# Optimization experiments

Measured on AMD Instinct MI355X. Metric: run time of the kernel, lower is better.

## Reference

```python
import jax, jax.numpy as jnp
import numpy as np
from jax import lax

KERNEL = 3
CIN = 512
FMAPS = 512
LATENT = 512
GAIN = 1.0
LRMUL = 1.0
# StyleGAN2 wscale: runtime_coef = gain / sqrt(fan_in) * lrmul
RC_W = GAIN / np.sqrt(KERNEL * KERNEL * CIN) * LRMUL
RC_S = GAIN / np.sqrt(LATENT) * LRMUL


def setup_inputs() -> dict:
    key = jax.random.key(0)
    k1, k2, k3, k4, k5 = jax.random.split(key, 5)
    N, H, W = 8, 64, 64
    x = jax.random.normal(k1, (N, CIN, H, W), dtype=jnp.float32)
    dlatent_vect = jax.random.normal(k2, (N, LATENT), dtype=jnp.float32)
    weight = jax.random.normal(k3, (KERNEL, KERNEL, CIN, FMAPS), dtype=jnp.float32)
    mod_weight = jax.random.normal(k4, (LATENT, CIN), dtype=jnp.float32)
    mod_bias = jax.random.normal(k5, (CIN,), dtype=jnp.float32)
    return {"x": x, "dlatent_vect": dlatent_vect, "weight": weight,
            "mod_weight": mod_weight, "mod_bias": mod_bias}


def reference(x, dlatent_vect, weight, mod_weight, mod_bias):
    N, _, H, W = x.shape
    w = weight * RC_W                                       # [kh,kw,Cin,Cout]
    # style: s = A(dlatent) + 1
    s = dlatent_vect @ (mod_weight * RC_S) + mod_bias * LRMUL + 1.0  # [N,Cin]
    # per-sample modulated weights
    ww = w[None] * s[:, None, None, :, None]                # [N,kh,kw,Cin,Cout]
    # demodulate
    d = lax.rsqrt(jnp.sum(jnp.square(ww), axis=(1, 2, 3)) + 1e-8)  # [N,Cout]
    ww = ww * d[:, None, None, None, :]
    # fused modconv: one grouped conv with N groups
    xr = x.reshape(1, N * CIN, H, W)
    wr = jnp.transpose(ww, (1, 2, 3, 0, 4)).reshape(KERNEL, KERNEL, CIN, N * FMAPS)
    out = lax.conv_general_dilated(
        xr, wr, window_strides=(1, 1), padding="SAME",
        dimension_numbers=("NCHW", "HWIO", "NCHW"),
        feature_group_count=N)
    return out.reshape(N, FMAPS, H, W)
```

## Files before the change

### kernel.cpp

```cpp
#include <hip/hip_runtime.h>
#include <math.h>

#define CIN_    512
#define COUT_   512
#define LATENT_ 512
#define NB_     8
#define HH_     64
#define WW_     64

typedef float f32x16 __attribute__((ext_vector_type(16)));
typedef short bf16x8v __attribute__((ext_vector_type(8)));

__device__ inline unsigned short f2bf(float f) {
    union { float f; unsigned u; } v; v.f = f;
    unsigned r = v.u + 0x7fffu + ((v.u >> 16) & 1u);
    return (unsigned short)(r >> 16);
}

__device__ __forceinline__ void gl_lds16(const void* g, void* l) {
    __builtin_amdgcn_global_load_lds(
        (const __attribute__((address_space(1))) unsigned int*)g,
        (__attribute__((address_space(3))) unsigned int*)l,
        16, 0, 0);
}

__global__ __launch_bounds__(256) void prep1(
    const float* __restrict__ w, const float* __restrict__ dlat,
    const float* __restrict__ mw, const float* __restrict__ mb,
    float* __restrict__ wsq, unsigned short* __restrict__ wb,
    float* __restrict__ s)
{
    __shared__ float smem[16 * 521];
    const float RC_W = 0.0147313912747197f;
    const float RC_S = 0.0441941738241592f;
    int b = blockIdx.x;
    int t = threadIdx.x;

    if (b < 1024) {
        int idx = b * 256 + t;
        float acc = 0.f;
#pragma unroll
        for (int tap = 0; tap < 9; ++tap) {
            float v = w[tap * (CIN_ * COUT_) + idx];
            acc += v * v;
        }
        wsq[idx] = acc;
    } else if (b < 1312) {
        int bb  = b - 1024;
        int tap = bb / 32;
        int cb  = bb % 32;
        for (int idx = t; idx < 16 * 512; idx += 256) {
            int ci = idx >> 9;
            int co = idx & 511;
            smem[ci * 521 + co] = w[((size_t)tap * 512 + cb * 16 + ci) * 512 + co];
        }
        __syncthreads();
        unsigned short* dst = wb + (size_t)(tap * 32 + cb) * 512 * 16;
        for (int idx = t; idx < 16 * 512; idx += 256) {
            int co = idx >> 4;
            int ci = idx & 15;
            dst[idx] = f2bf(smem[ci * 521 + co] * RC_W);
        }
    } else {
        int bb  = b - 1312;
        int n   = bb >> 3;
        int ci0 = (bb & 7) * 64;
        for (int i = t; i < LATENT_; i += 256) smem[i] = dlat[n * LATENT_ + i];
        __syncthreads();
        int cil  = t & 63;
        int part = t >> 6;
        const float* mwp = mw + ci0 + cil;
        float a0 = 0.f, a1 = 0.f;
        int l0 = part * 128;
#pragma unroll 4
        for (int l = l0; l < l0 + 128; l += 2) {
            a0 += smem[l]     * mwp[(size_t)l * CIN_];
            a1 += smem[l + 1] * mwp[(size_t)(l + 1) * CIN_];
        }
        smem[512 + part * 64 + cil] = a0 + a1;
        __syncthreads();
        if (t < 64) {
            float r = smem[512 + t] + smem[576 + t] + smem[640 + t] + smem[704 + t];
            s[n * CIN_ + ci0 + t] = r * RC_S + mb[ci0 + t] + 1.0f;
        }
    }
}

__global__ __launch_bounds__(256) void prep2(
    const float* __restrict__ x, const float* __restrict__ s,
    const float* __restrict__ wsq, float* __restrict__ dmod,
    unsigned short* __restrict__ xt)
{
    __shared__ float smem[16 * 67 + 16];
    int b = blockIdx.x;
    int t = threadIdx.x;

    if (b < 64) {
        const float RCW2 = 1.0f / 4608.0f;
        int n   = b >> 3;
        int co0 = (b & 7) * 64;
        for (int i = t; i < CIN_; i += 256) { float v = s[n * CIN_ + i]; smem[i] = v * v; }
        __syncthreads();
        int col  = t & 63;
        int part = t >> 6;
        const float* wp = wsq + co0 + col;
        float a0 = 0.f, a1 = 0.f;
        int c0 = part * 128;
#pragma unroll 4
        for (int ci = c0; ci < c0 + 128; ci += 2) {
            a0 += smem[ci]     * wp[(size_t)ci * COUT_];
            a1 += smem[ci + 1] * wp[(size_t)(ci + 1) * COUT_];
        }
        smem[512 + part * 64 + col] = a0 + a1;
        __syncthreads();
        if (t < 64) {
            float r = smem[512 + t] + smem[576 + t] + smem[640 + t] + smem[704 + t];
            dmod[n * COUT_ + co0 + t] = rsqrtf(RCW2 * r + 1e-8f);
        }
    } else {
        int bb = b - 64;
        int hp = bb % 66;
        int cb = (bb / 66) % 32;
        int n  = bb / (66 * 32);
        int gh = hp - 1;
        bool rowok = (gh >= 0) && (gh < HH_);

        if (t < 16) smem[16 * 67 + t] = s[n * CIN_ + cb * 16 + t];
        if (rowok) {
            const float* src = &x[(((size_t)n * CIN_ + cb * 16) * HH_ + gh) * WW_];
            int ci = t >> 4;
            int g0 = (t & 15) * 4;
            float4 v = *(const float4*)&src[(size_t)ci * (HH_ * WW_) + g0];
            float* dstl = &smem[ci * 67 + g0];
            dstl[0] = v.x; dstl[1] = v.y; dstl[2] = v.z; dstl[3] = v.w;
        }
        __syncthreads();

        unsigned short* dst = xt + (((size_t)(n * 32 + cb) * 66 + hp) * 66) * 16;
        for (int p = t; p < 264; p += 256) {
            int e   = p * 4;
            int wp_ = e >> 4;
            int cie = e & 15;
            int gw  = wp_ - 1;
            float vv0 = 0.f, vv1 = 0.f, vv2 = 0.f, vv3 = 0.f;
            if (rowok && gw >= 0 && gw < WW_) {
                vv0 = smem[(cie + 0) * 67 + gw] * smem[16 * 67 + cie + 0];
                vv1 = smem[(cie + 1) * 67 + gw] * smem[16 * 67 + cie + 1];
                vv2 = smem[(cie + 2) * 67 + gw] * smem[16 * 67 + cie + 2];
                vv3 = smem[(cie + 3) * 67 + gw] * smem[16 * 67 + cie + 3];
            }
            ushort4 o4;
            o4.x = f2bf(vv0); o4.y = f2bf(vv1); o4.z = f2bf(vv2); o4.w = f2bf(vv3);
            *(ushort4*)&dst[e] = o4;
        }
    }
}

__global__ __launch_bounds__(256, 2) void conv_mfma(
    const unsigned short* __restrict__ xt,
    const unsigned short* __restrict__ wb,
    const float* __restrict__ dmod,
    float* __restrict__ out)
{
    __shared__ __align__(16) union {
        struct { unsigned short xs[2880]; unsigned short ws[36864]; } s;
        float o[64 * 129];
    } sm;

    int b   = blockIdx.x;
    int cot = b & 1;
    int wt_ = (b >> 1) & 3;
    int ht  = (b >> 3) & 7;
    int n   = b >> 6;
    int h0 = ht * 8, w0 = wt_ * 16, co0 = cot * 256;

    int t    = threadIdx.x;
    int wv   = t >> 6, lane = t & 63;
    int mh   = wv >> 1, nh = wv & 1;
    int l5   = lane & 31, half = lane >> 5;

    f32x16 acc[2][4];
#pragma unroll
    for (int ms = 0; ms < 2; ++ms)
#pragma unroll
        for (int ns = 0; ns < 4; ++ns)
#pragma unroll
            for (int i = 0; i < 16; ++i) acc[ms][ns][i] = 0.f;

    for (int cb = 0; cb < 32; ++cb) {
        const unsigned short* xb = xt + (((size_t)(n * 32 + cb) * 66 + h0) * 66 + w0) * 16;
        {
            int li = t;
            gl_lds16(&xb[(li / 36) * 1056 + (li % 36) * 8], &sm.s.xs[(li - lane) * 8]);
            li = t + 256;
            if (li < 360)
                gl_lds16(&xb[(li / 36) * 1056 + (li % 36) * 8], &sm.s.xs[(li - lane) * 8]);
        }
        const unsigned short* wbb = wb + ((size_t)cb * 512 + co0) * 16;
#pragma unroll
        for (int tap = 0; tap < 9; ++tap) {
            const unsigned short* tsrc = wbb + (size_t)tap * 32 * 512 * 16;
            gl_lds16(&tsrc[t * 8],         &sm.s.ws[tap * 4096 + wv * 512]);
            gl_lds16(&tsrc[(t + 256) * 8], &sm.s.ws[tap * 4096 + 2048 + wv * 512]);
        }
        __syncthreads();

#pragma unroll
        for (int tap = 0; tap < 9; ++tap) {
            int kh = tap / 3, kw = tap - 3 * (tap / 3);
            bf16x8v bfr[4], afr[2];
#pragma unroll
            for (int ns = 0; ns < 4; ++ns) {
                int co_l = nh * 128 + ns * 32 + l5;
                bfr[ns] = *(const bf16x8v*)&sm.s.ws[tap * 4096 + co_l * 16 + half * 8];
            }
#pragma unroll
            for (int ms = 0; ms < 2; ++ms) {
                int pr = mh * 4 + ms * 2 + (l5 >> 4);
                int pc = l5 & 15;
                int pos = (pr + kh) * 18 + (pc + kw);
                afr[ms] = *(const bf16x8v*)&sm.s.xs[pos * 16 + half * 8];
            }
#pragma unroll
            for (int ms = 0; ms < 2; ++ms)
#pragma unroll
                for (int ns = 0; ns < 4; ++ns)
                    acc[ms][ns] = __builtin_amdgcn_mfma_f32_32x32x16_bf16(
                        afr[ms], bfr[ns], acc[ms][ns], 0, 0, 0);
        }
        __syncthreads();
    }

    for (int p = 0; p < 4; ++p) {
        __syncthreads();
        if (nh == (p >> 1)) {
#pragma unroll
            for (int q = 0; q < 2; ++q) {
                int bco = q * 32 + l5;
                float dv = dmod[n * COUT_ + co0 + p * 64 + bco];
#pragma unroll
                for (int ms = 0; ms < 2; ++ms) {
#pragma unroll
                    for (int reg = 0; reg < 16; ++reg) {
                        int ml = (reg & 3) + 8 * (reg >> 2) + 4 * half;
                        int m  = mh * 64 + ms * 32 + ml;
                        sm.o[bco * 129 + m] = acc[ms][(p & 1) * 2 + q][reg] * dv;
                    }
                }
            }
        }
        __syncthreads();
        for (int j = t; j < 2048; j += 256) {
            int wq = j & 3;
            int pairidx = j >> 2;
            int row  = pairidx & 7;
            int bco2 = pairidx >> 3;
            int co = co0 + p * 64 + bco2;
            const float* src = &sm.o[bco2 * 129 + row * 16 + wq * 4];
            float4 v = make_float4(src[0], src[1], src[2], src[3]);
            *(float4*)&out[(((size_t)n * COUT_ + co) * HH_ + h0 + row) * WW_ + w0 + wq * 4] = v;
        }
    }
}

extern "C" void kernel_launch(void* const* d_in, const int* in_sizes, int n_in,
                              void* d_out, int out_size, void* d_ws, size_t ws_size,
                              hipStream_t stream) {
    const float* x    = (const float*)d_in[0];
    const float* dlat = (const float*)d_in[1];
    const float* w    = (const float*)d_in[2];
    const float* mw   = (const float*)d_in[3];
    const float* mb   = (const float*)d_in[4];
    float* out = (float*)d_out;

    char* ws = (char*)d_ws;
    float* s    = (float*)(ws);
    float* dmod = (float*)(ws + 16384);
    float* wsq  = (float*)(ws + 32768);
    unsigned short* xt = (unsigned short*)(ws + 1081344);
    unsigned short* wb = (unsigned short*)(ws + 36765696);

    prep1<<<1376, 256, 0, stream>>>(w, dlat, mw, mb, wsq, wb, s);
    prep2<<<64 + NB_ * 32 * 66, 256, 0, stream>>>(x, s, wsq, dmod, xt);
    conv_mfma<<<512, 256, 0, stream>>>(xt, wb, dmod, out);
}
```

Measured before the change: 262.5 us.

## Swizzle LDS tiles, pre-permute weights to MFMA lane order, batch prep2 rows

The bf16 weight buffer is now written in MFMA fragment order (64 lanes × 8 ci per 32-co group), so each B-fragment LDS read is contiguous per lane and avoids bank conflicts. The activation tile in LDS gets an XOR swizzle on 16-byte chunks, applied both at the global-to-LDS load and at the A-fragment read, to reduce LDS bank conflicts. prep2 now has each block handle 11 padded rows instead of one, cutting the block count at the cost of extra barriers per row.

```diff
diff --git a/kernel.cpp b/kernel.cpp
--- a/kernel.cpp
+++ b/kernel.cpp
@@ -55,11 +55,18 @@
             smem[ci * 521 + co] = w[((size_t)tap * 512 + cb * 16 + ci) * 512 + co];
         }
         __syncthreads();
-        unsigned short* dst = wb + (size_t)(tap * 32 + cb) * 512 * 16;
-        for (int idx = t; idx < 16 * 512; idx += 256) {
-            int co = idx >> 4;
-            int ci = idx & 15;
-            dst[idx] = f2bf(smem[ci * 521 + co] * RC_W);
+        unsigned short* dst = wb + (size_t)(tap * 32 + cb) * 1024 * 8;
+        for (int p = t; p < 2048; p += 256) {
+            int l  = (p >> 1) & 63;
+            int g  = p >> 7;
+            int co = g * 32 + (l & 31);
+            int ci = (l >> 5) * 8 + (p & 1) * 4;
+            ushort4 o4;
+            o4.x = f2bf(smem[(ci + 0) * 521 + co] * RC_W);
+            o4.y = f2bf(smem[(ci + 1) * 521 + co] * RC_W);
+            o4.z = f2bf(smem[(ci + 2) * 521 + co] * RC_W);
+            o4.w = f2bf(smem[(ci + 3) * 521 + co] * RC_W);
+            *(ushort4*)&dst[p * 4] = o4;
         }
     } else {
         int bb  = b - 1312;
@@ -119,39 +126,43 @@
         }
     } else {
         int bb = b - 64;
-        int hp = bb % 66;
-        int cb = (bb / 66) % 32;
-        int n  = bb / (66 * 32);
-        int gh = hp - 1;
-        bool rowok = (gh >= 0) && (gh < HH_);
+        int rg = bb % 6;
+        int cb = (bb / 6) % 32;
+        int n  = bb / (6 * 32);
 
         if (t < 16) smem[16 * 67 + t] = s[n * CIN_ + cb * 16 + t];
-        if (rowok) {
-            const float* src = &x[(((size_t)n * CIN_ + cb * 16) * HH_ + gh) * WW_];
-            int ci = t >> 4;
-            int g0 = (t & 15) * 4;
-            float4 v = *(const float4*)&src[(size_t)ci * (HH_ * WW_) + g0];
-            float* dstl = &smem[ci * 67 + g0];
-            dstl[0] = v.x; dstl[1] = v.y; dstl[2] = v.z; dstl[3] = v.w;
-        }
-        __syncthreads();
-
-        unsigned short* dst = xt + (((size_t)(n * 32 + cb) * 66 + hp) * 66) * 16;
-        for (int p = t; p < 264; p += 256) {
-            int e   = p * 4;
-            int wp_ = e >> 4;
-            int cie = e & 15;
-            int gw  = wp_ - 1;
-            float vv0 = 0.f, vv1 = 0.f, vv2 = 0.f, vv3 = 0.f;
-            if (rowok && gw >= 0 && gw < WW_) {
-                vv0 = smem[(cie + 0) * 67 + gw] * smem[16 * 67 + cie + 0];
-                vv1 = smem[(cie + 1) * 67 + gw] * smem[16 * 67 + cie + 1];
-                vv2 = smem[(cie + 2) * 67 + gw] * smem[16 * 67 + cie + 2];
-                vv3 = smem[(cie + 3) * 67 + gw] * smem[16 * 67 + cie + 3];
-            }
-            ushort4 o4;
-            o4.x = f2bf(vv0); o4.y = f2bf(vv1); o4.z = f2bf(vv2); o4.w = f2bf(vv3);
-            *(ushort4*)&dst[e] = o4;
+
+        for (int hp = rg * 11; hp < rg * 11 + 11; ++hp) {
+            int gh = hp - 1;
+            bool rowok = (gh >= 0) && (gh < HH_);
+            if (rowok) {
+                const float* src = &x[(((size_t)n * CIN_ + cb * 16) * HH_ + gh) * WW_];
+                int ci = t >> 4;
+                int g0 = (t & 15) * 4;
+                float4 v = *(const float4*)&src[(size_t)ci * (HH_ * WW_) + g0];
+                float* dstl = &smem[ci * 67 + g0];
+                dstl[0] = v.x; dstl[1] = v.y; dstl[2] = v.z; dstl[3] = v.w;
+            }
+            __syncthreads();
+
+            unsigned short* dst = xt + (((size_t)(n * 32 + cb) * 66 + hp) * 66) * 16;
+            for (int p = t; p < 264; p += 256) {
+                int e   = p * 4;
+                int wp_ = e >> 4;
+                int cie = e & 15;
+                int gw  = wp_ - 1;
+                float vv0 = 0.f, vv1 = 0.f, vv2 = 0.f, vv3 = 0.f;
+                if (rowok && gw >= 0 && gw < WW_) {
+                    vv0 = smem[(cie + 0) * 67 + gw] * smem[16 * 67 + cie + 0];
+                    vv1 = smem[(cie + 1) * 67 + gw] * smem[16 * 67 + cie + 1];
+                    vv2 = smem[(cie + 2) * 67 + gw] * smem[16 * 67 + cie + 2];
+                    vv3 = smem[(cie + 3) * 67 + gw] * smem[16 * 67 + cie + 3];
+                }
+                ushort4 o4;
+                o4.x = f2bf(vv0); o4.y = f2bf(vv1); o4.z = f2bf(vv2); o4.w = f2bf(vv3);
+                *(ushort4*)&dst[e] = o4;
+            }
+            __syncthreads();
         }
     }
 }
@@ -191,17 +202,20 @@
         const unsigned short* xb = xt + (((size_t)(n * 32 + cb) * 66 + h0) * 66 + w0) * 16;
         {
             int li = t;
-            gl_lds16(&xb[(li / 36) * 1056 + (li % 36) * 8], &sm.s.xs[(li - lane) * 8]);
+            int m  = li ^ ((li >> 3) & 7);
+            gl_lds16(&xb[(m / 36) * 1056 + (m % 36) * 8], &sm.s.xs[(li & ~63) * 8]);
             li = t + 256;
-            if (li < 360)
-                gl_lds16(&xb[(li / 36) * 1056 + (li % 36) * 8], &sm.s.xs[(li - lane) * 8]);
-        }
-        const unsigned short* wbb = wb + ((size_t)cb * 512 + co0) * 16;
+            if (li < 360) {
+                m = li ^ ((li >> 3) & 7);
+                gl_lds16(&xb[(m / 36) * 1056 + (m % 36) * 8], &sm.s.xs[(li & ~63) * 8]);
+            }
+        }
+        const unsigned short* wbb = wb + ((size_t)cb * 1024 + cot * 512) * 8;
 #pragma unroll
         for (int tap = 0; tap < 9; ++tap) {
-            const unsigned short* tsrc = wbb + (size_t)tap * 32 * 512 * 16;
-            gl_lds16(&tsrc[t * 8],         &sm.s.ws[tap * 4096 + wv * 512]);
-            gl_lds16(&tsrc[(t + 256) * 8], &sm.s.ws[tap * 4096 + 2048 + wv * 512]);
+            const unsigned short* tsrc = wbb + (size_t)tap * 32 * 1024 * 8;
+            gl_lds16(&tsrc[t * 8],         &sm.s.ws[tap * 4096 + (t & ~63) * 8]);
+            gl_lds16(&tsrc[(t + 256) * 8], &sm.s.ws[tap * 4096 + ((t + 256) & ~63) * 8]);
         }
         __syncthreads();
 
@@ -211,15 +225,16 @@
             bf16x8v bfr[4], afr[2];
 #pragma unroll
             for (int ns = 0; ns < 4; ++ns) {
-                int co_l = nh * 128 + ns * 32 + l5;
-                bfr[ns] = *(const bf16x8v*)&sm.s.ws[tap * 4096 + co_l * 16 + half * 8];
+                bfr[ns] = *(const bf16x8v*)&sm.s.ws[tap * 4096 + ((nh * 4 + ns) * 64 + lane) * 8];
             }
 #pragma unroll
             for (int ms = 0; ms < 2; ++ms) {
                 int pr = mh * 4 + ms * 2 + (l5 >> 4);
                 int pc = l5 & 15;
                 int pos = (pr + kh) * 18 + (pc + kw);
-                afr[ms] = *(const bf16x8v*)&sm.s.xs[pos * 16 + half * 8];
+                int ch  = pos * 2 + half;
+                ch ^= (ch >> 3) & 7;
+                afr[ms] = *(const bf16x8v*)&sm.s.xs[ch * 8];
             }
 #pragma unroll
             for (int ms = 0; ms < 2; ++ms)
@@ -281,6 +296,6 @@
     unsigned short* wb = (unsigned short*)(ws + 36765696);
 
     prep1<<<1376, 256, 0, stream>>>(w, dlat, mw, mb, wsq, wb, s);
-    prep2<<<64 + NB_ * 32 * 66, 256, 0, stream>>>(x, s, wsq, dmod, xt);
+    prep2<<<64 + NB_ * 32 * 6, 256, 0, stream>>>(x, s, wsq, dmod, xt);
     conv_mfma<<<512, 256, 0, stream>>>(xt, wb, dmod, out);
 }
```

New measurement: 264.6 us. Within noise of the previous version (+0.8%).
